# Kernel tuning notes

Measured on AMD Instinct MI355X. Metric: run time of the kernel, lower is better.

Reference implementation:

```python
import jax, jax.numpy as jnp
import numpy as np

D_MODEL = 768
H = 12
D_K = D_MODEL // H
NEG = -1e9


def setup_inputs() -> dict:
    key = jax.random.key(0)
    ks = jax.random.split(key, 12)
    B, S = 1, 4096
    q = jax.random.normal(ks[0], (B, S, D_MODEL), dtype=jnp.float32)
    k = jax.random.normal(ks[1], (B, S, D_MODEL), dtype=jnp.float32)
    v = jax.random.normal(ks[2], (B, S, D_MODEL), dtype=jnp.float32)
    # causal mask, 1 = attend, 0 = masked (masked_fill on mask == 0)
    mask = jnp.tril(jnp.ones((S, S), dtype=jnp.int32))[None, None, :, :]
    scale = 1.0 / np.sqrt(D_MODEL)
    Wq = jax.random.normal(ks[3], (D_MODEL, D_MODEL), dtype=jnp.float32) * scale
    bq = jnp.zeros((D_MODEL,), dtype=jnp.float32)
    Wk = jax.random.normal(ks[4], (D_MODEL, D_MODEL), dtype=jnp.float32) * scale
    bk = jnp.zeros((D_MODEL,), dtype=jnp.float32)
    Wv = jax.random.normal(ks[5], (D_MODEL, D_MODEL), dtype=jnp.float32) * scale
    bv = jnp.zeros((D_MODEL,), dtype=jnp.float32)
    Wo = jax.random.normal(ks[6], (D_MODEL, D_MODEL), dtype=jnp.float32) * scale
    bo = jnp.zeros((D_MODEL,), dtype=jnp.float32)
    return {"q": q, "k": k, "v": v, "mask": mask,
            "Wq": Wq, "bq": bq, "Wk": Wk, "bk": bk,
            "Wv": Wv, "bv": bv, "Wo": Wo, "bo": bo}


def _split_heads(x):
    B, S, _ = x.shape
    return x.reshape(B, S, H, D_K).transpose(0, 2, 1, 3)  # [B,H,S,Dk]


def reference(q, k, v, mask, Wq, bq, Wk, bk, Wv, bv, Wo, bo):
    # Linear projections (torch Linear: x @ W.T + b; here W stored as [in,out])
    query = _split_heads(q @ Wq + bq)
    key = _split_heads(k @ Wk + bk)
    value = _split_heads(v @ Wv + bv)
    # scaled dot-product attention, full score matrix [B,H,Sq,Sk]
    scores = jnp.einsum("bhqd,bhkd->bhqk", query, key) / jnp.sqrt(
        jnp.asarray(D_K, dtype=query.dtype))
    scores = jnp.where(mask == 0, jnp.asarray(NEG, dtype=scores.dtype), scores)
    attn = jax.nn.softmax(scores, axis=-1)  # dropout p=0.0 -> identity
    x = jnp.einsum("bhqk,bhkd->bhqd", attn, value)
    B, _, S, _ = x.shape
    x = x.transpose(0, 2, 1, 3).reshape(B, S, H * D_K)
    return x @ Wo + bo
```

## Files before the change

kernel.cpp:

```cpp
#include <hip/hip_runtime.h>

typedef __bf16 bf16;
typedef __bf16 bf16x4 __attribute__((ext_vector_type(4)));
typedef __bf16 bf16x8 __attribute__((ext_vector_type(8)));
typedef float  floatx4 __attribute__((ext_vector_type(4)));

#define MFMA16(a,b,c) __builtin_amdgcn_mfma_f32_16x16x32_bf16((a),(b),(c),0,0,0)

static constexpr int S_LEN = 4096;
static constexpr int DM = 768;
static constexpr int NH = 12;
static constexpr int W_ELEMS = 768 * 768;
static constexpr int PARTS_PER_HEAD = 144;
static constexpr float CE = 0.18033688011112042f;

__device__ __forceinline__ void gld16(const bf16* g, bf16* l) {
    __builtin_amdgcn_global_load_lds(
        (const __attribute__((address_space(1))) void*)g,
        (__attribute__((address_space(3))) void*)l, 16, 0, 0);
}

__global__ __launch_bounds__(256) void prep_kernel(
    const float* __restrict__ q, const float* __restrict__ k, const float* __restrict__ v,
    const float* __restrict__ W0, const float* __restrict__ W1,
    const float* __restrict__ W2, const float* __restrict__ W3,
    bf16* Qc, bf16* Kc, bf16* Vc,
    bf16* T0, bf16* T1, bf16* T2, bf16* T3, int n)
{
    const int y = blockIdx.y;
    const int tid = threadIdx.x;
    if (y < 3) {
        const float* src = y == 0 ? q : (y == 1 ? k : v);
        bf16* dst = y == 0 ? Qc : (y == 1 ? Kc : Vc);
        int i = (blockIdx.x * 256 + tid) * 4;
        if (i < n) {
            float4 w = *(const float4*)&src[i];
            bf16x4 o; o[0] = (bf16)w.x; o[1] = (bf16)w.y; o[2] = (bf16)w.z; o[3] = (bf16)w.w;
            *(bf16x4*)&dst[i] = o;
        }
        return;
    }
    int x = blockIdx.x;
    if (x >= 576) return;
    const int mat = x / 144, t = x % 144;
    const float* W = mat == 0 ? W0 : (mat == 1 ? W1 : (mat == 2 ? W2 : W3));
    bf16* T = mat == 0 ? T0 : (mat == 1 ? T1 : (mat == 2 ? T2 : T3));
    const int k0 = (t / 12) * 64, n0 = (t % 12) * 64;
    __shared__ float Tl[64][65];
#pragma unroll
    for (int i = 0; i < 4; ++i) {
        int idx = i * 256 + tid;
        int r = idx >> 4, c4 = idx & 15;
        float4 w = *(const float4*)&W[(k0 + r) * 768 + n0 + c4 * 4];
        Tl[c4 * 4 + 0][r] = w.x; Tl[c4 * 4 + 1][r] = w.y;
        Tl[c4 * 4 + 2][r] = w.z; Tl[c4 * 4 + 3][r] = w.w;
    }
    __syncthreads();
#pragma unroll
    for (int i = 0; i < 4; ++i) {
        int idx = i * 256 + tid;
        int c = idx >> 4, r4 = idx & 15;
        bf16x4 o;
        o[0] = (bf16)Tl[c][r4 * 4 + 0]; o[1] = (bf16)Tl[c][r4 * 4 + 1];
        o[2] = (bf16)Tl[c][r4 * 4 + 2]; o[3] = (bf16)Tl[c][r4 * 4 + 3];
        *(bf16x4*)&T[(n0 + c) * 768 + k0 + r4 * 4] = o;
    }
}

__global__ __launch_bounds__(256) void vtrans_kernel(
    const bf16* __restrict__ Vp, bf16* __restrict__ VpT)
{
    __shared__ bf16 Tl[64][66];
    const int tid = threadIdx.x;
    const int r0 = blockIdx.x * 64, c0 = blockIdx.y * 64;
#pragma unroll
    for (int i = 0; i < 4; ++i) {
        int idx = i * 256 + tid;
        int r = idx >> 4, c4 = idx & 15;
        bf16x4 w = *(const bf16x4*)&Vp[(size_t)(r0 + r) * DM + c0 + c4 * 4];
        Tl[c4 * 4 + 0][r] = w[0]; Tl[c4 * 4 + 1][r] = w[1];
        Tl[c4 * 4 + 2][r] = w[2]; Tl[c4 * 4 + 3][r] = w[3];
    }
    __syncthreads();
#pragma unroll
    for (int i = 0; i < 4; ++i) {
        int idx = i * 256 + tid;
        int c = idx >> 4, r4 = idx & 15;
        bf16x4 o;
        o[0] = Tl[c][r4 * 4 + 0]; o[1] = Tl[c][r4 * 4 + 1];
        o[2] = Tl[c][r4 * 4 + 2]; o[3] = Tl[c][r4 * 4 + 3];
        *(bf16x4*)&VpT[(size_t)(c0 + c) * S_LEN + r0 + r4 * 4] = o;
    }
}

template <bool OUT_F32>
__global__ __launch_bounds__(256) void gemm128_kernel(
    const bf16* __restrict__ A0, const bf16* __restrict__ A1, const bf16* __restrict__ A2,
    const bf16* __restrict__ B0, const bf16* __restrict__ B1, const bf16* __restrict__ B2,
    const float* __restrict__ c0, const float* __restrict__ c1, const float* __restrict__ c2,
    void* O0, void* O1, void* O2, int M, int N, int K, float qscale)
{
    const int z = blockIdx.z;
    const bf16* A = z == 0 ? A0 : (z == 1 ? A1 : A2);
    const bf16* B = z == 0 ? B0 : (z == 1 ? B1 : B2);
    const float* bias = z == 0 ? c0 : (z == 1 ? c1 : c2);
    void* C = z == 0 ? O0 : (z == 1 ? O1 : O2);
    const float osc = (z == 0) ? qscale : 1.0f;

    __shared__ bf16 As[2][128 * 64];
    __shared__ bf16 Bs[2][128 * 64];
    const int tid = threadIdx.x, lane = tid & 63, wave = tid >> 6;
    const int quad = lane >> 4, l16 = lane & 15, l8 = l16 & 7;
    const int rw = wave >> 1, cw = wave & 1;
    const int m0 = blockIdx.x * 128, n0 = blockIdx.y * 128;

    floatx4 acc[4][4] = {};

    auto stage = [&](int kt, int buf) {
#pragma unroll
        for (int i = 0; i < 4; ++i) {
            int ch = i * 256 + tid;
            int m = ch >> 3, kg = ch & 7;
            int kgd = kg ^ (m & 7);
            gld16(A + (size_t)(m0 + m) * K + kt * 64 + kgd * 8, &As[buf][ch * 8]);
        }
#pragma unroll
        for (int i = 0; i < 4; ++i) {
            int ch = i * 256 + tid;
            int n = ch >> 3, kg = ch & 7;
            int kgd = kg ^ (n & 7);
            gld16(B + (size_t)(n0 + n) * K + kt * 64 + kgd * 8, &Bs[buf][ch * 8]);
        }
    };

    const int NT = K >> 6;
    stage(0, 0);
    __syncthreads();

    for (int kt = 0; kt < NT; ++kt) {
        const int cur = kt & 1;
        if (kt + 1 < NT) stage(kt + 1, cur ^ 1);
#pragma unroll
        for (int ks = 0; ks < 2; ++ks) {
            bf16x8 a[4], b[4];
#pragma unroll
            for (int mt = 0; mt < 4; ++mt)
                a[mt] = *(const bf16x8*)&As[cur][(rw * 64 + mt * 16 + l16) * 64 + (((ks * 4 + quad) ^ l8) << 3)];
#pragma unroll
            for (int nt = 0; nt < 4; ++nt)
                b[nt] = *(const bf16x8*)&Bs[cur][(cw * 64 + nt * 16 + l16) * 64 + (((ks * 4 + quad) ^ l8) << 3)];
#pragma unroll
            for (int mt = 0; mt < 4; ++mt)
#pragma unroll
                for (int nt = 0; nt < 4; ++nt)
                    acc[mt][nt] = MFMA16(a[mt], b[nt], acc[mt][nt]);
        }
        __syncthreads();
    }
#pragma unroll
    for (int mt = 0; mt < 4; ++mt) {
        int row = m0 + rw * 64 + mt * 16 + quad * 4;
#pragma unroll
        for (int nt = 0; nt < 4; ++nt) {
            int col = n0 + cw * 64 + nt * 16 + l16;
            float bv = bias[col];
#pragma unroll
            for (int r = 0; r < 4; ++r) {
                float v = (acc[mt][nt][r] + bv) * osc;
                if (OUT_F32) ((float*)C)[(size_t)(row + r) * N + col] = v;
                else         ((bf16*)C)[(size_t)(row + r) * N + col] = (bf16)v;
            }
        }
    }
}

__global__ __launch_bounds__(256) void attn_kernel(
    const bf16* __restrict__ Q, const bf16* __restrict__ K,
    const bf16* __restrict__ VpT, bf16* __restrict__ Opart,
    float* __restrict__ Lpart)
{
    __shared__ bf16 Ps[128 * 64];
    __shared__ bf16 Ks[2][64 * 64];
    __shared__ bf16 Vt[2][64 * 64];

    const int h = blockIdx.y;
    const int idx = PARTS_PER_HEAD - 1 - (int)blockIdx.x;
    int g = 0;
    while (2 * (g + 1) * (g + 2) <= idx) ++g;
    const int rem = idx - 2 * g * (g + 1);
    const int qb = 4 * g + rem / (g + 1);
    const int c  = rem % (g + 1);
    const int ntiles = 2 * qb + 2;
    const int jstart = c * 8;
    const int jend   = (jstart + 8 < ntiles) ? jstart + 8 : ntiles;

    const int tid = threadIdx.x, lane = tid & 63, wave = tid >> 6;
    const int quad = lane >> 4, l16 = lane & 15, l8 = l16 & 7;
    const int qrow0 = qb * 128;
    const int cb = h * 64;

    auto stageKV = [&](int j, int buf) {
#pragma unroll
        for (int i = 0; i < 2; ++i) {
            int ch = i * 256 + tid;
            int row = ch >> 3, kg = ch & 7;
            int kgd = kg ^ (row & 7);
            gld16(K + (size_t)(j * 64 + row) * DM + cb + kgd * 8, &Ks[buf][ch * 8]);
        }
#pragma unroll
        for (int i = 0; i < 2; ++i) {
            int ch = i * 256 + tid;
            int row = ch >> 3, kg = ch & 7;
            int kgd = kg ^ (row & 7);
            gld16(VpT + (size_t)(cb + row) * S_LEN + j * 64 + kgd * 8, &Vt[buf][ch * 8]);
        }
    };

    bf16x8 qreg[2][2];
#pragma unroll
    for (int mt = 0; mt < 2; ++mt)
#pragma unroll
        for (int ks = 0; ks < 2; ++ks)
            qreg[mt][ks] = *(const bf16x8*)&Q[(size_t)(qrow0 + wave * 32 + mt * 16 + l16) * DM
                                             + cb + ks * 32 + quad * 8];

    stageKV(jstart, 0);
    __syncthreads();

    floatx4 o[2][4] = {};
    float lsum[2] = {0.f, 0.f};
    const int prowbase = (wave * 32 + l16) * 64;
    const int psub = (quad & 1) * 4;
    const int c16base = (quad >> 1);

    for (int j = jstart; j < jend; ++j) {
        const int cur = (j - jstart) & 1;
        if (j + 1 < jend) stageKV(j + 1, cur ^ 1);

        floatx4 st[2][4] = {};
#pragma unroll
        for (int ks = 0; ks < 2; ++ks) {
            bf16x8 kfr[4];
#pragma unroll
            for (int ct = 0; ct < 4; ++ct)
                kfr[ct] = *(const bf16x8*)&Ks[cur][(ct * 16 + l16) * 64 + (((ks * 4 + quad) ^ l8) << 3)];
#pragma unroll
            for (int mt = 0; mt < 2; ++mt)
#pragma unroll
                for (int ct = 0; ct < 4; ++ct)
                    st[mt][ct] = MFMA16(kfr[ct], qreg[mt][ks], st[mt][ct]);
        }

#pragma unroll
        for (int mt = 0; mt < 2; ++mt) {
            const int qs0 = qrow0 + wave * 32 + mt * 16;
            const int pb = prowbase + mt * 16 * 64;
            float lp = 0.f;
            if ((j * 64 + 63) <= qs0) {
#pragma unroll
                for (int ct = 0; ct < 4; ++ct) {
                    bf16x4 pk;
#pragma unroll
                    for (int r = 0; r < 4; ++r) {
                        float p = __builtin_amdgcn_exp2f(st[mt][ct][r]);
                        lp += p; pk[r] = (bf16)p;
                    }
                    *(bf16x4*)&Ps[pb + ((((ct * 2 + c16base) ^ l8) << 3) + psub)] = pk;
                }
            } else {
                const int qg = qs0 + l16;
#pragma unroll
                for (int ct = 0; ct < 4; ++ct) {
                    const int kg0 = j * 64 + ct * 16 + quad * 4;
                    bf16x4 pk;
#pragma unroll
                    for (int r = 0; r < 4; ++r) {
                        float p = (kg0 + r > qg) ? 0.f
                                  : __builtin_amdgcn_exp2f(st[mt][ct][r]);
                        lp += p; pk[r] = (bf16)p;
                    }
                    *(bf16x4*)&Ps[pb + ((((ct * 2 + c16base) ^ l8) << 3) + psub)] = pk;
                }
            }
            lsum[mt] += lp;
        }

#pragma unroll
        for (int ks = 0; ks < 2; ++ks) {
            bf16x8 bfr[4], afr[2];
#pragma unroll
            for (int ct = 0; ct < 4; ++ct)
                bfr[ct] = *(const bf16x8*)&Vt[cur][(ct * 16 + l16) * 64 + (((ks * 4 + quad) ^ l8) << 3)];
#pragma unroll
            for (int mt = 0; mt < 2; ++mt)
                afr[mt] = *(const bf16x8*)&Ps[(wave * 32 + mt * 16 + l16) * 64 + (((ks * 4 + quad) ^ l8) << 3)];
#pragma unroll
            for (int mt = 0; mt < 2; ++mt)
#pragma unroll
                for (int ct = 0; ct < 4; ++ct)
                    o[mt][ct] = MFMA16(afr[mt], bfr[ct], o[mt][ct]);
        }

        __syncthreads();
    }

    bf16* Op = Opart + (size_t)(h * PARTS_PER_HEAD + idx) * 128 * 64;
    float* Lp = Lpart + (size_t)(h * PARTS_PER_HEAD + idx) * 128;
#pragma unroll
    for (int mt = 0; mt < 2; ++mt) {
        float l = lsum[mt];
        l += __shfl_xor(l, 16);
        l += __shfl_xor(l, 32);
        if (lane < 16) Lp[wave * 32 + mt * 16 + l16] = l;
#pragma unroll
        for (int r = 0; r < 4; ++r) {
            const int rl = wave * 32 + mt * 16 + quad * 4 + r;
#pragma unroll
            for (int ct = 0; ct < 4; ++ct)
                Op[rl * 64 + ct * 16 + l16] = (bf16)o[mt][ct][r];
        }
    }
}

__global__ __launch_bounds__(256) void attn_combine_kernel(
    const bf16* __restrict__ Opart, const float* __restrict__ Lpart,
    bf16* __restrict__ X)
{
    const int qb = blockIdx.x, h = blockIdx.y;
    const int g = qb >> 2;
    const int nc = g + 1;
    const int base = 2 * g * (g + 1) + (qb & 3) * (g + 1);
    const bf16* Op0 = Opart + (size_t)(h * PARTS_PER_HEAD + base) * 128 * 64;
    const float* Lp0 = Lpart + (size_t)(h * PARTS_PER_HEAD + base) * 128;

    for (int e = threadIdx.x * 4; e < 128 * 64; e += 1024) {
        const int row = e >> 6, col = e & 63;
        float4 acc = {0.f, 0.f, 0.f, 0.f};
        float l = 0.f;
        for (int p = 0; p < nc; ++p) {
            bf16x4 w = *(const bf16x4*)&Op0[p * 128 * 64 + e];
            acc.x += (float)w[0]; acc.y += (float)w[1];
            acc.z += (float)w[2]; acc.w += (float)w[3];
            l += Lp0[p * 128 + row];
        }
        const float rl = 1.0f / l;
        bf16x4 ov;
        ov[0] = (bf16)(acc.x * rl); ov[1] = (bf16)(acc.y * rl);
        ov[2] = (bf16)(acc.z * rl); ov[3] = (bf16)(acc.w * rl);
        *(bf16x4*)&X[(size_t)(qb * 128 + row) * DM + h * 64 + col] = ov;
    }
}

extern "C" void kernel_launch(void* const* d_in, const int* in_sizes, int n_in,
                              void* d_out, int out_size, void* d_ws, size_t ws_size,
                              hipStream_t stream)
{
    const float* q  = (const float*)d_in[0];
    const float* k  = (const float*)d_in[1];
    const float* v  = (const float*)d_in[2];
    const float* Wq = (const float*)d_in[4];
    const float* bq = (const float*)d_in[5];
    const float* Wk = (const float*)d_in[6];
    const float* bk = (const float*)d_in[7];
    const float* Wv = (const float*)d_in[8];
    const float* bv = (const float*)d_in[9];
    const float* Wo = (const float*)d_in[10];
    const float* bo = (const float*)d_in[11];

    const size_t NE = (size_t)S_LEN * DM;
    bf16* base = (bf16*)d_ws;
    bf16* Qp = base;
    bf16* Kp = base + NE;
    bf16* Vp = base + 2 * NE;
    bf16* Wt = base + 3 * NE;
    bf16 *Wqt = Wt, *Wkt = Wt + W_ELEMS, *Wvt = Wt + 2 * W_ELEMS, *Wot = Wt + 3 * W_ELEMS;
    bf16* VpT = Wt + 4 * W_ELEMS;
    bf16* scratch = VpT + NE;
    bf16* Qc = scratch;
    bf16* Kc = scratch + NE;
    bf16* Vc = scratch + 2 * NE;
    bf16* Opart = scratch;
    float* Lpart = (float*)(Opart + (size_t)NH * PARTS_PER_HEAD * 128 * 64);
    bf16* Xb = Qp;

    prep_kernel<<<dim3(3072, 4), 256, 0, stream>>>(
        q, k, v, Wq, Wk, Wv, Wo, Qc, Kc, Vc, Wqt, Wkt, Wvt, Wot, (int)NE);
    gemm128_kernel<false><<<dim3(32, 6, 3), 256, 0, stream>>>(
        Qc, Kc, Vc, Wqt, Wkt, Wvt, bq, bk, bv, Qp, Kp, Vp, S_LEN, DM, DM, CE);
    vtrans_kernel<<<dim3(64, 12), 256, 0, stream>>>(Vp, VpT);
    attn_kernel<<<dim3(PARTS_PER_HEAD, NH), 256, 0, stream>>>(Qp, Kp, VpT, Opart, Lpart);
    attn_combine_kernel<<<dim3(32, NH), 256, 0, stream>>>(Opart, Lpart, Xb);
    gemm128_kernel<true><<<dim3(32, 6, 1), 256, 0, stream>>>(
        Xb, Xb, Xb, Wot, Wot, Wot, bo, bo, bo, d_out, d_out, d_out, S_LEN, DM, DM, 1.0f);
}
```

Baseline: 260.6 us.

## Fuse V transpose into projection GEMM epilogue and shrink GEMM tile to 128x64

Removes the separate V transpose kernel by having the V projection GEMM write its output directly in transposed [D, S] layout from the epilogue. The GEMM tile is also reduced from 128x128 to 128x64, with the grid reordered so N is the fast dimension, which doubles the block count for better CU occupancy on the 4096x768 problems. The cost is lower per-block data reuse and more A-tile reloads, plus strided 8-byte stores for the transposed output.

New measurement: 257.5 us. No clear change (-1.2%).

```diff
diff --git a/kernel.cpp b/kernel.cpp
--- a/kernel.cpp
+++ b/kernel.cpp
@@ -67,34 +67,8 @@
     }
 }
 
-__global__ __launch_bounds__(256) void vtrans_kernel(
-    const bf16* __restrict__ Vp, bf16* __restrict__ VpT)
-{
-    __shared__ bf16 Tl[64][66];
-    const int tid = threadIdx.x;
-    const int r0 = blockIdx.x * 64, c0 = blockIdx.y * 64;
-#pragma unroll
-    for (int i = 0; i < 4; ++i) {
-        int idx = i * 256 + tid;
-        int r = idx >> 4, c4 = idx & 15;
-        bf16x4 w = *(const bf16x4*)&Vp[(size_t)(r0 + r) * DM + c0 + c4 * 4];
-        Tl[c4 * 4 + 0][r] = w[0]; Tl[c4 * 4 + 1][r] = w[1];
-        Tl[c4 * 4 + 2][r] = w[2]; Tl[c4 * 4 + 3][r] = w[3];
-    }
-    __syncthreads();
-#pragma unroll
-    for (int i = 0; i < 4; ++i) {
-        int idx = i * 256 + tid;
-        int c = idx >> 4, r4 = idx & 15;
-        bf16x4 o;
-        o[0] = Tl[c][r4 * 4 + 0]; o[1] = Tl[c][r4 * 4 + 1];
-        o[2] = Tl[c][r4 * 4 + 2]; o[3] = Tl[c][r4 * 4 + 3];
-        *(bf16x4*)&VpT[(size_t)(c0 + c) * S_LEN + r0 + r4 * 4] = o;
-    }
-}
-
-template <bool OUT_F32>
-__global__ __launch_bounds__(256) void gemm128_kernel(
+template <bool OUT_F32, bool VT_Z2>
+__global__ __launch_bounds__(256) void gemm_kernel(
     const bf16* __restrict__ A0, const bf16* __restrict__ A1, const bf16* __restrict__ A2,
     const bf16* __restrict__ B0, const bf16* __restrict__ B1, const bf16* __restrict__ B2,
     const float* __restrict__ c0, const float* __restrict__ c1, const float* __restrict__ c2,
@@ -108,13 +82,13 @@
     const float osc = (z == 0) ? qscale : 1.0f;
 
     __shared__ bf16 As[2][128 * 64];
-    __shared__ bf16 Bs[2][128 * 64];
+    __shared__ bf16 Bs[2][64 * 64];
     const int tid = threadIdx.x, lane = tid & 63, wave = tid >> 6;
     const int quad = lane >> 4, l16 = lane & 15, l8 = l16 & 7;
     const int rw = wave >> 1, cw = wave & 1;
-    const int m0 = blockIdx.x * 128, n0 = blockIdx.y * 128;
-
-    floatx4 acc[4][4] = {};
+    const int n0 = blockIdx.x * 64, m0 = blockIdx.y * 128;
+
+    floatx4 acc[4][2] = {};
 
     auto stage = [&](int kt, int buf) {
 #pragma unroll
@@ -125,7 +99,7 @@
             gld16(A + (size_t)(m0 + m) * K + kt * 64 + kgd * 8, &As[buf][ch * 8]);
         }
 #pragma unroll
-        for (int i = 0; i < 4; ++i) {
+        for (int i = 0; i < 2; ++i) {
             int ch = i * 256 + tid;
             int n = ch >> 3, kg = ch & 7;
             int kgd = kg ^ (n & 7);
@@ -142,27 +116,44 @@
         if (kt + 1 < NT) stage(kt + 1, cur ^ 1);
 #pragma unroll
         for (int ks = 0; ks < 2; ++ks) {
-            bf16x8 a[4], b[4];
+            bf16x8 a[4], b[2];
 #pragma unroll
             for (int mt = 0; mt < 4; ++mt)
                 a[mt] = *(const bf16x8*)&As[cur][(rw * 64 + mt * 16 + l16) * 64 + (((ks * 4 + quad) ^ l8) << 3)];
 #pragma unroll
-            for (int nt = 0; nt < 4; ++nt)
-                b[nt] = *(const bf16x8*)&Bs[cur][(cw * 64 + nt * 16 + l16) * 64 + (((ks * 4 + quad) ^ l8) << 3)];
+            for (int nt = 0; nt < 2; ++nt)
+                b[nt] = *(const bf16x8*)&Bs[cur][(cw * 32 + nt * 16 + l16) * 64 + (((ks * 4 + quad) ^ l8) << 3)];
 #pragma unroll
             for (int mt = 0; mt < 4; ++mt)
 #pragma unroll
-                for (int nt = 0; nt < 4; ++nt)
+                for (int nt = 0; nt < 2; ++nt)
                     acc[mt][nt] = MFMA16(a[mt], b[nt], acc[mt][nt]);
         }
         __syncthreads();
+    }
+
+    if (VT_Z2 && z == 2) {
+#pragma unroll
+        for (int mt = 0; mt < 4; ++mt) {
+            int row = m0 + rw * 64 + mt * 16 + quad * 4;
+#pragma unroll
+            for (int nt = 0; nt < 2; ++nt) {
+                int col = n0 + cw * 32 + nt * 16 + l16;
+                float bv = bias[col];
+                bf16x4 pk;
+#pragma unroll
+                for (int r = 0; r < 4; ++r) pk[r] = (bf16)(acc[mt][nt][r] + bv);
+                *(bf16x4*)&((bf16*)C)[(size_t)col * S_LEN + row] = pk;
+            }
+        }
+        return;
     }
 #pragma unroll
     for (int mt = 0; mt < 4; ++mt) {
         int row = m0 + rw * 64 + mt * 16 + quad * 4;
 #pragma unroll
-        for (int nt = 0; nt < 4; ++nt) {
-            int col = n0 + cw * 64 + nt * 16 + l16;
+        for (int nt = 0; nt < 2; ++nt) {
+            int col = n0 + cw * 32 + nt * 16 + l16;
             float bv = bias[col];
 #pragma unroll
             for (int r = 0; r < 4; ++r) {
@@ -369,13 +360,12 @@
 
     const size_t NE = (size_t)S_LEN * DM;
     bf16* base = (bf16*)d_ws;
-    bf16* Qp = base;
-    bf16* Kp = base + NE;
-    bf16* Vp = base + 2 * NE;
-    bf16* Wt = base + 3 * NE;
+    bf16* Qp  = base;
+    bf16* Kp  = base + NE;
+    bf16* VpT = base + 2 * NE;
+    bf16* Wt  = base + 3 * NE;
     bf16 *Wqt = Wt, *Wkt = Wt + W_ELEMS, *Wvt = Wt + 2 * W_ELEMS, *Wot = Wt + 3 * W_ELEMS;
-    bf16* VpT = Wt + 4 * W_ELEMS;
-    bf16* scratch = VpT + NE;
+    bf16* scratch = Wt + 4 * W_ELEMS;
     bf16* Qc = scratch;
     bf16* Kc = scratch + NE;
     bf16* Vc = scratch + 2 * NE;
@@ -385,11 +375,10 @@
 
     prep_kernel<<<dim3(3072, 4), 256, 0, stream>>>(
         q, k, v, Wq, Wk, Wv, Wo, Qc, Kc, Vc, Wqt, Wkt, Wvt, Wot, (int)NE);
-    gemm128_kernel<false><<<dim3(32, 6, 3), 256, 0, stream>>>(
-        Qc, Kc, Vc, Wqt, Wkt, Wvt, bq, bk, bv, Qp, Kp, Vp, S_LEN, DM, DM, CE);
-    vtrans_kernel<<<dim3(64, 12), 256, 0, stream>>>(Vp, VpT);
+    gemm_kernel<false, true><<<dim3(12, 32, 3), 256, 0, stream>>>(
+        Qc, Kc, Vc, Wqt, Wkt, Wvt, bq, bk, bv, Qp, Kp, VpT, S_LEN, DM, DM, CE);
     attn_kernel<<<dim3(PARTS_PER_HEAD, NH), 256, 0, stream>>>(Qp, Kp, VpT, Opart, Lpart);
     attn_combine_kernel<<<dim3(32, NH), 256, 0, stream>>>(Opart, Lpart, Xb);
-    gemm128_kernel<true><<<dim3(32, 6, 1), 256, 0, stream>>>(
+    gemm_kernel<true, false><<<dim3(12, 32, 1), 256, 0, stream>>>(
         Xb, Xb, Xb, Wot, Wot, Wot, bo, bo, bo, d_out, d_out, d_out, S_LEN, DM, DM, 1.0f);
 }
```
